# Performance work log

Hardware: AMD Instinct MI355X
Metric: run time of the kernel (lower is better)

The kernel has to match this reference:

```python
import jax, jax.numpy as jnp
import numpy as np

EMBED_DIM = 1024
N_HEADS = 16
HEAD_DIM = EMBED_DIM // N_HEADS
CHUNK = 64  # reward_data_gen_params['chunk_size']
B, T = 8, 1024


def setup_inputs() -> dict:
    key = jax.random.key(0)
    ks = jax.random.split(key, 9)
    s = 0.02
    return {
        "x": jax.random.normal(ks[0], (B, T, EMBED_DIM), dtype=jnp.float32),
        "Wq": jax.random.normal(ks[1], (EMBED_DIM, EMBED_DIM), dtype=jnp.float32) * s,
        "bq": jax.random.normal(ks[2], (EMBED_DIM,), dtype=jnp.float32) * s,
        "Wk": jax.random.normal(ks[3], (EMBED_DIM, EMBED_DIM), dtype=jnp.float32) * s,
        "bk": jax.random.normal(ks[4], (EMBED_DIM,), dtype=jnp.float32) * s,
        "Wv": jax.random.normal(ks[5], (EMBED_DIM, EMBED_DIM), dtype=jnp.float32) * s,
        "bv": jax.random.normal(ks[6], (EMBED_DIM,), dtype=jnp.float32) * s,
        "Wo": jax.random.normal(ks[7], (EMBED_DIM, EMBED_DIM), dtype=jnp.float32) * s,
        "bo": jax.random.normal(ks[8], (EMBED_DIM,), dtype=jnp.float32) * s,
        "attn_scale": jnp.full((1,), 1.0 / np.sqrt(HEAD_DIM), dtype=jnp.float32),
    }


def reference(x, Wq, bq, Wk, bk, Wv, bv, Wo, bo, attn_scale):
    Bsz, Tlen, C = x.shape
    H, D = N_HEADS, HEAD_DIM
    # torch Linear: y = x @ W.T + b
    q = (x @ Wq.T + bq).reshape(Bsz, Tlen, H, D).transpose(0, 2, 1, 3)  # [B,H,T,D]
    k = (x @ Wk.T + bk).reshape(Bsz, Tlen, H, D).transpose(0, 2, 1, 3)
    v = (x @ Wv.T + bv).reshape(Bsz, Tlen, H, D).transpose(0, 2, 1, 3)

    scores = jnp.einsum("bhqd,bhkd->bhqk", q, k) * attn_scale[0]  # [B,H,T,T]

    # Faithful reproduction of the chunked masking: the source only masks when
    # query-chunk >= key-chunk, which (given key>query implies key-chunk>=query-chunk)
    # reduces to masking key>query ONLY inside diagonal CHUNK x CHUNK blocks.
    idx = jnp.arange(Tlen)
    same_block = (idx[:, None] // CHUNK) == (idx[None, :] // CHUNK)
    mask = (idx[None, :] > idx[:, None]) & same_block  # [T,T] True => masked
    scores = jnp.where(mask[None, None], -jnp.inf, scores)

    w = jax.nn.softmax(scores, axis=-1)
    out = jnp.einsum("bhqk,bhkd->bhqd", w, v)  # [B,H,T,D]
    out = out.transpose(0, 2, 1, 3).reshape(Bsz, Tlen, C)
    return out @ Wo.T + bo
```

## Files before the change

### kernel.cpp

```cpp
#include <hip/hip_runtime.h>


typedef __bf16 bf16;
typedef __bf16 bf16x8 __attribute__((ext_vector_type(8)));
typedef float  f32x4  __attribute__((ext_vector_type(4)));

#define LOG2E 1.44269504088896340736f

__device__ __forceinline__ void async16(const bf16* g, bf16* l) {
  __builtin_amdgcn_global_load_lds(
      (const __attribute__((address_space(1))) void*)g,
      (__attribute__((address_space(3))) void*)l, 16, 0, 0);
}

#if __has_builtin(__builtin_amdgcn_exp2f)
#define EXP2F(x) __builtin_amdgcn_exp2f(x)
#else
#define EXP2F(x) exp2f(x)
#endif

__global__ __launch_bounds__(256) void k_convert(
    const float* __restrict__ x, const float* __restrict__ wq,
    const float* __restrict__ wk, const float* __restrict__ wv,
    const float* __restrict__ wo, bf16* __restrict__ xb, bf16* __restrict__ wb) {
  const int XV = (8192 * 1024) / 4;
  const int WV = (1024 * 1024) / 4;
  int i = blockIdx.x * 256 + threadIdx.x;
  const float4* src;
  bf16* dst;
  if (i < XV) {
    src = (const float4*)x + i;
    dst = xb + (size_t)i * 4;
  } else {
    int j = i - XV;
    int w = j >> 18;
    int r = j & (WV - 1);
    const float* s = (w == 0) ? wq : (w == 1) ? wk : (w == 2) ? wv : wo;
    src = (const float4*)s + r;
    dst = wb + (size_t)w * (1024 * 1024) + (size_t)r * 4;
  }
  float4 f = *src;
  bf16 tmp[4] = {(bf16)f.x, (bf16)f.y, (bf16)f.z, (bf16)f.w};
  *(uint2*)dst = *(uint2*)tmp;
}

__global__ __launch_bounds__(256) void k_gemm_qkv(
    const bf16* __restrict__ A, const bf16* __restrict__ W,
    const float* __restrict__ bq, const float* __restrict__ bk,
    const float* __restrict__ bv, const float* __restrict__ scale_p,
    bf16* __restrict__ qb, bf16* __restrict__ kb, bf16* __restrict__ vb) {
  __shared__ __attribute__((aligned(16))) bf16 As[2][4096];
  __shared__ __attribute__((aligned(16))) bf16 Bs[2][4096];
  const int tid = threadIdx.x, lane = tid & 63, wid = tid >> 6;
  const int quad = lane >> 4, l16 = lane & 15;
  const int wm = (wid & 1) * 64, wn = (wid >> 1) * 64;
  const int tileM = blockIdx.x * 128, tileN = blockIdx.y * 128;

  const int rql = lane >> 2;
  const int lc = (lane & 3) ^ ((lane >> 3) & 3);
  const bf16* Ap = A + (size_t)(tileM + wid * 16 + rql) * 1024 + lc * 8;
  const bf16* Bp = W + (size_t)(tileN + wid * 16 + rql) * 1024 + lc * 8;
  const int wofs = wid * 512;

  f32x4 acc[4][4];
#pragma unroll
  for (int i = 0; i < 4; i++)
#pragma unroll
    for (int j = 0; j < 4; j++) acc[i][j] = (f32x4){0.f, 0.f, 0.f, 0.f};

  async16(Ap, &As[0][wofs]);
  async16(Ap + 64 * 1024, &As[0][2048 + wofs]);
  async16(Bp, &Bs[0][wofs]);
  async16(Bp + 64 * 1024, &Bs[0][2048 + wofs]);

  for (int it = 0; it < 32; it++) {
    const int pp = it & 1;
    __syncthreads();
    if (it < 31) {
      int k0 = (it + 1) * 32;
      async16(Ap + k0, &As[pp ^ 1][wofs]);
      async16(Ap + k0 + 64 * 1024, &As[pp ^ 1][2048 + wofs]);
      async16(Bp + k0, &Bs[pp ^ 1][wofs]);
      async16(Bp + k0 + 64 * 1024, &Bs[pp ^ 1][2048 + wofs]);
    }
    bf16x8 af[4], bfr[4];
#pragma unroll
    for (int i = 0; i < 4; i++) {
      int r = wm + i * 16 + l16;
      af[i] = *(const bf16x8*)&As[pp][r * 32 + ((quad ^ ((r >> 1) & 3)) * 8)];
    }
#pragma unroll
    for (int j = 0; j < 4; j++) {
      int r = wn + j * 16 + l16;
      bfr[j] = *(const bf16x8*)&Bs[pp][r * 32 + ((quad ^ ((r >> 1) & 3)) * 8)];
    }
#pragma unroll
    for (int i = 0; i < 4; i++)
#pragma unroll
      for (int j = 0; j < 4; j++)
        acc[i][j] = __builtin_amdgcn_mfma_f32_16x16x32_bf16(af[i], bfr[j], acc[i][j], 0, 0, 0);
  }

  float qscale = scale_p[0] * LOG2E;
#pragma unroll
  for (int i = 0; i < 4; i++) {
    int m0 = tileM + wm + i * 16 + quad * 4;
    int b = m0 >> 10;
    int t0 = m0 & 1023;
#pragma unroll
    for (int j = 0; j < 4; j++) {
      int n = tileN + wn + j * 16 + l16;
      int which = n >> 10;
      int nm = n & 1023;
      int h = nm >> 6, d = nm & 63;
      float bias = ((which == 0) ? bq : (which == 1) ? bk : bv)[nm];
      if (which == 2) {
        bf16 tmp[4];
#pragma unroll
        for (int r = 0; r < 4; r++) tmp[r] = (bf16)(acc[i][j][r] + bias);
        size_t vidx = (((size_t)((b * 16 + h) * 64 + d)) << 10) | (size_t)t0;
        *(uint2*)&vb[vidx] = *(uint2*)tmp;
      } else {
#pragma unroll
        for (int r = 0; r < 4; r++) {
          float v = acc[i][j][r] + bias;
          size_t idx = (((size_t)(b * 16 + h) * 1024 + (t0 + r)) << 6) | (size_t)d;
          if (which == 0) qb[idx] = (bf16)(v * qscale);
          else            kb[idx] = (bf16)v;
        }
      }
    }
  }
}

__global__ __launch_bounds__(256) void k_gemm_out(
    const bf16* __restrict__ A, const bf16* __restrict__ W,
    const float* __restrict__ bo, float* __restrict__ out) {
  __shared__ __attribute__((aligned(16))) bf16 As[2][4096];
  __shared__ __attribute__((aligned(16))) bf16 Bs[2][4096];
  const int tid = threadIdx.x, lane = tid & 63, wid = tid >> 6;
  const int quad = lane >> 4, l16 = lane & 15;
  const int wm = (wid & 1) * 64, wn = (wid >> 1) * 64;
  const int tileM = blockIdx.x * 128, tileN = blockIdx.y * 128;

  const int rql = lane >> 2;
  const int lc = (lane & 3) ^ ((lane >> 3) & 3);
  const bf16* Ap = A + (size_t)(tileM + wid * 16 + rql) * 1024 + lc * 8;
  const bf16* Bp = W + (size_t)(tileN + wid * 16 + rql) * 1024 + lc * 8;
  const int wofs = wid * 512;

  f32x4 acc[4][4];
#pragma unroll
  for (int i = 0; i < 4; i++)
#pragma unroll
    for (int j = 0; j < 4; j++) acc[i][j] = (f32x4){0.f, 0.f, 0.f, 0.f};

  async16(Ap, &As[0][wofs]);
  async16(Ap + 64 * 1024, &As[0][2048 + wofs]);
  async16(Bp, &Bs[0][wofs]);
  async16(Bp + 64 * 1024, &Bs[0][2048 + wofs]);

  for (int it = 0; it < 32; it++) {
    const int pp = it & 1;
    __syncthreads();
    if (it < 31) {
      int k0 = (it + 1) * 32;
      async16(Ap + k0, &As[pp ^ 1][wofs]);
      async16(Ap + k0 + 64 * 1024, &As[pp ^ 1][2048 + wofs]);
      async16(Bp + k0, &Bs[pp ^ 1][wofs]);
      async16(Bp + k0 + 64 * 1024, &Bs[pp ^ 1][2048 + wofs]);
    }
    bf16x8 af[4], bfr[4];
#pragma unroll
    for (int i = 0; i < 4; i++) {
      int r = wm + i * 16 + l16;
      af[i] = *(const bf16x8*)&As[pp][r * 32 + ((quad ^ ((r >> 1) & 3)) * 8)];
    }
#pragma unroll
    for (int j = 0; j < 4; j++) {
      int r = wn + j * 16 + l16;
      bfr[j] = *(const bf16x8*)&Bs[pp][r * 32 + ((quad ^ ((r >> 1) & 3)) * 8)];
    }
#pragma unroll
    for (int i = 0; i < 4; i++)
#pragma unroll
      for (int j = 0; j < 4; j++)
        acc[i][j] = __builtin_amdgcn_mfma_f32_16x16x32_bf16(af[i], bfr[j], acc[i][j], 0, 0, 0);
  }

#pragma unroll
  for (int i = 0; i < 4; i++)
#pragma unroll
    for (int j = 0; j < 4; j++) {
      int n = tileN + wn + j * 16 + l16;
      float bias = bo[n];
#pragma unroll
      for (int r = 0; r < 4; r++) {
        int m = tileM + wm + i * 16 + quad * 4 + r;
        out[(size_t)m * 1024 + n] = acc[i][j][r] + bias;
      }
    }
}

__global__ __launch_bounds__(256, 2) void k_attn(
    const bf16* __restrict__ qb, const bf16* __restrict__ kb,
    const bf16* __restrict__ vb, bf16* __restrict__ attn) {
  __shared__ __attribute__((aligned(16))) bf16 KsF[2][4096];
  __shared__ __attribute__((aligned(16))) bf16 VsF[2][4096];
  __shared__ __attribute__((aligned(16))) bf16 Pl[4][4][16][72];
  const int tid = threadIdx.x, lane = tid & 63, wid = tid >> 6;
  const int quad = lane >> 4, l16 = lane & 15;
  const int bh = blockIdx.x;
  const int qt = blockIdx.y;
  const size_t base = (size_t)bh * (1024 * 64);
  const int qrow0 = qt * 256;

  bf16x8 qf[4][2];
#pragma unroll
  for (int s = 0; s < 4; s++) {
    const bf16* qrow = qb + base + (size_t)(qrow0 + s * 64 + wid * 16 + l16) * 64;
    qf[s][0] = *(const bf16x8*)(qrow + quad * 8);
    qf[s][1] = *(const bf16x8*)(qrow + 32 + quad * 8);
  }

  f32x4 oacc[4][4], lacc[4];
#pragma unroll
  for (int s = 0; s < 4; s++) {
    lacc[s] = (f32x4){0.f, 0.f, 0.f, 0.f};
#pragma unroll
    for (int j = 0; j < 4; j++) oacc[s][j] = (f32x4){0.f, 0.f, 0.f, 0.f};
  }

  bf16x8 ones;
#pragma unroll
  for (int e = 0; e < 8; e++) ones[e] = (bf16)1.0f;

  const int krow = lane >> 3;
  const int klc = (lane & 7) ^ krow;
  const bf16* kp = kb + base + (size_t)(wid * 8 + krow) * 64 + klc * 8;
  const bf16* vp = vb + base + (size_t)(wid * 8 + krow) * 1024 + klc * 8;
  const int wofs = wid * 512;

  async16(kp, &KsF[0][wofs]);
  async16(kp + 32 * 64, &KsF[0][2048 + wofs]);
  async16(vp, &VsF[0][wofs]);
  async16(vp + 32 * 1024, &VsF[0][2048 + wofs]);

  const int sw = l16 & 7;
  for (int kt = 0; kt < 16; kt++) {
    const int pp = kt & 1;
    __syncthreads();

    if (kt < 15) {
      const bf16* kpn = kp + (size_t)(kt + 1) * 4096;
      const bf16* vpn = vp + (size_t)(kt + 1) * 64;
      async16(kpn, &KsF[pp ^ 1][wofs]);
      async16(kpn + 32 * 64, &KsF[pp ^ 1][2048 + wofs]);
      async16(vpn, &VsF[pp ^ 1][wofs]);
      async16(vpn + 32 * 1024, &VsF[pp ^ 1][2048 + wofs]);
    }

    bf16x8 kf[4][2];
#pragma unroll
    for (int j = 0; j < 4; j++) {
      int row = (j * 16 + l16) * 64;
      kf[j][0] = *(const bf16x8*)&KsF[pp][row + ((quad ^ sw) * 8)];
      kf[j][1] = *(const bf16x8*)&KsF[pp][row + (((quad + 4) ^ sw) * 8)];
    }
#pragma unroll
    for (int s = 0; s < 4; s++) {
      f32x4 sv[4];
#pragma unroll
      for (int j = 0; j < 4; j++) {
        f32x4 z = (f32x4){0.f, 0.f, 0.f, 0.f};
        z = __builtin_amdgcn_mfma_f32_16x16x32_bf16(qf[s][0], kf[j][0], z, 0, 0, 0);
        z = __builtin_amdgcn_mfma_f32_16x16x32_bf16(qf[s][1], kf[j][1], z, 0, 0, 0);
        sv[j] = z;
      }
      if (qt * 4 + s == kt) {
#pragma unroll
        for (int j = 0; j < 4; j++) {
          int kpos = j * 16 + l16;
#pragma unroll
          for (int r = 0; r < 4; r++) {
            int qpos = wid * 16 + quad * 4 + r;
            if (kpos > qpos) sv[j][r] = -1e30f;
          }
        }
      }
#pragma unroll
      for (int j = 0; j < 4; j++)
#pragma unroll
        for (int r = 0; r < 4; r++)
          Pl[wid][s][quad * 4 + r][j * 16 + l16] = (bf16)EXP2F(sv[j][r]);
    }

#pragma unroll
    for (int ks = 0; ks < 2; ks++) {
      bf16x8 vf[4];
#pragma unroll
      for (int j = 0; j < 4; j++) {
        int row = (j * 16 + l16) * 64;
        vf[j] = *(const bf16x8*)&VsF[pp][row + (((ks * 4 + quad) ^ sw) * 8)];
      }
#pragma unroll
      for (int s = 0; s < 4; s++) {
        bf16x8 pf = *(const bf16x8*)&Pl[wid][s][l16][ks * 32 + quad * 8];
#pragma unroll
        for (int j = 0; j < 4; j++)
          oacc[s][j] = __builtin_amdgcn_mfma_f32_16x16x32_bf16(pf, vf[j], oacc[s][j], 0, 0, 0);
        lacc[s] = __builtin_amdgcn_mfma_f32_16x16x32_bf16(pf, ones, lacc[s], 0, 0, 0);
      }
    }
  }

  const int b = bh >> 4, h = bh & 15;
#pragma unroll
  for (int s = 0; s < 4; s++) {
    float inv[4];
#pragma unroll
    for (int r = 0; r < 4; r++) inv[r] = 1.0f / lacc[s][r];
#pragma unroll
    for (int j = 0; j < 4; j++)
#pragma unroll
      for (int r = 0; r < 4; r++) {
        int qg = qrow0 + s * 64 + wid * 16 + quad * 4 + r;
        float o = oacc[s][j][r] * inv[r];
        attn[((size_t)(b * 1024 + qg) << 10) + h * 64 + j * 16 + l16] = (bf16)o;
      }
  }
}

extern "C" void kernel_launch(void* const* d_in, const int* in_sizes, int n_in,
                              void* d_out, int out_size, void* d_ws, size_t ws_size,
                              hipStream_t stream) {
  const float* x     = (const float*)d_in[0];
  const float* Wq    = (const float*)d_in[1];
  const float* bq    = (const float*)d_in[2];
  const float* Wk    = (const float*)d_in[3];
  const float* bk    = (const float*)d_in[4];
  const float* Wv    = (const float*)d_in[5];
  const float* bv    = (const float*)d_in[6];
  const float* Wo    = (const float*)d_in[7];
  const float* bo    = (const float*)d_in[8];
  const float* scale = (const float*)d_in[9];

  char* ws = (char*)d_ws;
  bf16* xb   = (bf16*)(ws);
  bf16* wb   = (bf16*)(ws + (size_t)(16 << 20));
  bf16* qb   = (bf16*)(ws + (size_t)(24 << 20));
  bf16* kb   = (bf16*)(ws + (size_t)(40 << 20));
  bf16* vb   = (bf16*)(ws + (size_t)(56 << 20));
  bf16* attn = xb;
  float* out = (float*)d_out;

  hipLaunchKernelGGL(k_convert, dim3(12288), dim3(256), 0, stream,
                     x, Wq, Wk, Wv, Wo, xb, wb);
  hipLaunchKernelGGL(k_gemm_qkv, dim3(64, 24), dim3(256), 0, stream,
                     xb, wb, bq, bk, bv, scale, qb, kb, vb);
  hipLaunchKernelGGL(k_attn, dim3(128, 4), dim3(256), 0, stream,
                     qb, kb, vb, attn);
  hipLaunchKernelGGL(k_gemm_out, dim3(64, 8), dim3(256), 0, stream,
                     attn, wb + (size_t)3072 * 1024, bo, out);
}
```

Baseline: 252.6 us.

## Keep attention P in registers via transposed MFMA and widen GEMM K-tile

The attention kernel now computes S^T by swapping the MFMA operands. The exponentiated probabilities then land directly in the B-operand register layout for the PV product. This removes the shared-memory P round trip and the extra ones-MFMA used for row sums, which are replaced by register sums plus cross-lane shuffles, and the output stores become 4-wide. The two GEMMs switch from a double-buffered 32-wide K tile to a single-buffered 64-wide K tile with two barriers per iteration, which removes prefetch overlap in exchange for fewer iterations and a new swizzle.

```diff
diff --git a/kernel.cpp b/kernel.cpp
--- a/kernel.cpp
+++ b/kernel.cpp
@@ -2,6 +2,7 @@
 
 
 typedef __bf16 bf16;
+typedef __bf16 bf16x4 __attribute__((ext_vector_type(4)));
 typedef __bf16 bf16x8 __attribute__((ext_vector_type(8)));
 typedef float  f32x4  __attribute__((ext_vector_type(4)));
 
@@ -49,18 +50,19 @@
     const float* __restrict__ bq, const float* __restrict__ bk,
     const float* __restrict__ bv, const float* __restrict__ scale_p,
     bf16* __restrict__ qb, bf16* __restrict__ kb, bf16* __restrict__ vb) {
-  __shared__ __attribute__((aligned(16))) bf16 As[2][4096];
-  __shared__ __attribute__((aligned(16))) bf16 Bs[2][4096];
+  __shared__ __attribute__((aligned(16))) bf16 As[8192];
+  __shared__ __attribute__((aligned(16))) bf16 Bs[8192];
   const int tid = threadIdx.x, lane = tid & 63, wid = tid >> 6;
   const int quad = lane >> 4, l16 = lane & 15;
   const int wm = (wid & 1) * 64, wn = (wid >> 1) * 64;
   const int tileM = blockIdx.x * 128, tileN = blockIdx.y * 128;
 
-  const int rql = lane >> 2;
-  const int lc = (lane & 3) ^ ((lane >> 3) & 3);
-  const bf16* Ap = A + (size_t)(tileM + wid * 16 + rql) * 1024 + lc * 8;
-  const bf16* Bp = W + (size_t)(tileN + wid * 16 + rql) * 1024 + lc * 8;
+  const int krow = lane >> 3;
+  const int gc = (lane & 7) ^ krow;
+  const bf16* Ap = A + (size_t)(tileM + wid * 8 + krow) * 1024 + gc * 8;
+  const bf16* Bp = W + (size_t)(tileN + wid * 8 + krow) * 1024 + gc * 8;
   const int wofs = wid * 512;
+  const int s7 = l16 & 7;
 
   f32x4 acc[4][4];
 #pragma unroll
@@ -68,37 +70,31 @@
 #pragma unroll
     for (int j = 0; j < 4; j++) acc[i][j] = (f32x4){0.f, 0.f, 0.f, 0.f};
 
-  async16(Ap, &As[0][wofs]);
-  async16(Ap + 64 * 1024, &As[0][2048 + wofs]);
-  async16(Bp, &Bs[0][wofs]);
-  async16(Bp + 64 * 1024, &Bs[0][2048 + wofs]);
-
-  for (int it = 0; it < 32; it++) {
-    const int pp = it & 1;
-    __syncthreads();
-    if (it < 31) {
-      int k0 = (it + 1) * 32;
-      async16(Ap + k0, &As[pp ^ 1][wofs]);
-      async16(Ap + k0 + 64 * 1024, &As[pp ^ 1][2048 + wofs]);
-      async16(Bp + k0, &Bs[pp ^ 1][wofs]);
-      async16(Bp + k0 + 64 * 1024, &Bs[pp ^ 1][2048 + wofs]);
-    }
-    bf16x8 af[4], bfr[4];
-#pragma unroll
-    for (int i = 0; i < 4; i++) {
-      int r = wm + i * 16 + l16;
-      af[i] = *(const bf16x8*)&As[pp][r * 32 + ((quad ^ ((r >> 1) & 3)) * 8)];
-    }
-#pragma unroll
-    for (int j = 0; j < 4; j++) {
-      int r = wn + j * 16 + l16;
-      bfr[j] = *(const bf16x8*)&Bs[pp][r * 32 + ((quad ^ ((r >> 1) & 3)) * 8)];
-    }
-#pragma unroll
-    for (int i = 0; i < 4; i++)
+  for (int it = 0; it < 16; it++) {
+    const int k0 = it * 64;
+#pragma unroll
+    for (int rd = 0; rd < 4; rd++) {
+      async16(Ap + (size_t)rd * 32768 + k0, &As[rd * 2048 + wofs]);
+      async16(Bp + (size_t)rd * 32768 + k0, &Bs[rd * 2048 + wofs]);
+    }
+    __syncthreads();
+#pragma unroll
+    for (int kh = 0; kh < 2; kh++) {
+      const int pc = ((kh * 4 + quad) ^ s7) * 8;
+      bf16x8 af[4], bfr[4];
+#pragma unroll
+      for (int i = 0; i < 4; i++)
+        af[i] = *(const bf16x8*)&As[(wm + i * 16 + l16) * 64 + pc];
 #pragma unroll
       for (int j = 0; j < 4; j++)
-        acc[i][j] = __builtin_amdgcn_mfma_f32_16x16x32_bf16(af[i], bfr[j], acc[i][j], 0, 0, 0);
+        bfr[j] = *(const bf16x8*)&Bs[(wn + j * 16 + l16) * 64 + pc];
+#pragma unroll
+      for (int i = 0; i < 4; i++)
+#pragma unroll
+        for (int j = 0; j < 4; j++)
+          acc[i][j] = __builtin_amdgcn_mfma_f32_16x16x32_bf16(af[i], bfr[j], acc[i][j], 0, 0, 0);
+    }
+    __syncthreads();
   }
 
   float qscale = scale_p[0] * LOG2E;
@@ -136,18 +132,19 @@
 __global__ __launch_bounds__(256) void k_gemm_out(
     const bf16* __restrict__ A, const bf16* __restrict__ W,
     const float* __restrict__ bo, float* __restrict__ out) {
-  __shared__ __attribute__((aligned(16))) bf16 As[2][4096];
-  __shared__ __attribute__((aligned(16))) bf16 Bs[2][4096];
+  __shared__ __attribute__((aligned(16))) bf16 As[8192];
+  __shared__ __attribute__((aligned(16))) bf16 Bs[8192];
   const int tid = threadIdx.x, lane = tid & 63, wid = tid >> 6;
   const int quad = lane >> 4, l16 = lane & 15;
   const int wm = (wid & 1) * 64, wn = (wid >> 1) * 64;
   const int tileM = blockIdx.x * 128, tileN = blockIdx.y * 128;
 
-  const int rql = lane >> 2;
-  const int lc = (lane & 3) ^ ((lane >> 3) & 3);
-  const bf16* Ap = A + (size_t)(tileM + wid * 16 + rql) * 1024 + lc * 8;
-  const bf16* Bp = W + (size_t)(tileN + wid * 16 + rql) * 1024 + lc * 8;
+  const int krow = lane >> 3;
+  const int gc = (lane & 7) ^ krow;
+  const bf16* Ap = A + (size_t)(tileM + wid * 8 + krow) * 1024 + gc * 8;
+  const bf16* Bp = W + (size_t)(tileN + wid * 8 + krow) * 1024 + gc * 8;
   const int wofs = wid * 512;
+  const int s7 = l16 & 7;
 
   f32x4 acc[4][4];
 #pragma unroll
@@ -155,37 +152,31 @@
 #pragma unroll
     for (int j = 0; j < 4; j++) acc[i][j] = (f32x4){0.f, 0.f, 0.f, 0.f};
 
-  async16(Ap, &As[0][wofs]);
-  async16(Ap + 64 * 1024, &As[0][2048 + wofs]);
-  async16(Bp, &Bs[0][wofs]);
-  async16(Bp + 64 * 1024, &Bs[0][2048 + wofs]);
-
-  for (int it = 0; it < 32; it++) {
-    const int pp = it & 1;
-    __syncthreads();
-    if (it < 31) {
-      int k0 = (it + 1) * 32;
-      async16(Ap + k0, &As[pp ^ 1][wofs]);
-      async16(Ap + k0 + 64 * 1024, &As[pp ^ 1][2048 + wofs]);
-      async16(Bp + k0, &Bs[pp ^ 1][wofs]);
-      async16(Bp + k0 + 64 * 1024, &Bs[pp ^ 1][2048 + wofs]);
-    }
-    bf16x8 af[4], bfr[4];
-#pragma unroll
-    for (int i = 0; i < 4; i++) {
-      int r = wm + i * 16 + l16;
-      af[i] = *(const bf16x8*)&As[pp][r * 32 + ((quad ^ ((r >> 1) & 3)) * 8)];
-    }
-#pragma unroll
-    for (int j = 0; j < 4; j++) {
-      int r = wn + j * 16 + l16;
-      bfr[j] = *(const bf16x8*)&Bs[pp][r * 32 + ((quad ^ ((r >> 1) & 3)) * 8)];
-    }
-#pragma unroll
-    for (int i = 0; i < 4; i++)
+  for (int it = 0; it < 16; it++) {
+    const int k0 = it * 64;
+#pragma unroll
+    for (int rd = 0; rd < 4; rd++) {
+      async16(Ap + (size_t)rd * 32768 + k0, &As[rd * 2048 + wofs]);
+      async16(Bp + (size_t)rd * 32768 + k0, &Bs[rd * 2048 + wofs]);
+    }
+    __syncthreads();
+#pragma unroll
+    for (int kh = 0; kh < 2; kh++) {
+      const int pc = ((kh * 4 + quad) ^ s7) * 8;
+      bf16x8 af[4], bfr[4];
+#pragma unroll
+      for (int i = 0; i < 4; i++)
+        af[i] = *(const bf16x8*)&As[(wm + i * 16 + l16) * 64 + pc];
 #pragma unroll
       for (int j = 0; j < 4; j++)
-        acc[i][j] = __builtin_amdgcn_mfma_f32_16x16x32_bf16(af[i], bfr[j], acc[i][j], 0, 0, 0);
+        bfr[j] = *(const bf16x8*)&Bs[(wn + j * 16 + l16) * 64 + pc];
+#pragma unroll
+      for (int i = 0; i < 4; i++)
+#pragma unroll
+        for (int j = 0; j < 4; j++)
+          acc[i][j] = __builtin_amdgcn_mfma_f32_16x16x32_bf16(af[i], bfr[j], acc[i][j], 0, 0, 0);
+    }
+    __syncthreads();
   }
 
 #pragma unroll
@@ -207,7 +198,6 @@
     const bf16* __restrict__ vb, bf16* __restrict__ attn) {
   __shared__ __attribute__((aligned(16))) bf16 KsF[2][4096];
   __shared__ __attribute__((aligned(16))) bf16 VsF[2][4096];
-  __shared__ __attribute__((aligned(16))) bf16 Pl[4][4][16][72];
   const int tid = threadIdx.x, lane = tid & 63, wid = tid >> 6;
   const int quad = lane >> 4, l16 = lane & 15;
   const int bh = blockIdx.x;
@@ -223,17 +213,14 @@
     qf[s][1] = *(const bf16x8*)(qrow + 32 + quad * 8);
   }
 
-  f32x4 oacc[4][4], lacc[4];
+  f32x4 oacc[4][4];
+  float lpart[4];
 #pragma unroll
   for (int s = 0; s < 4; s++) {
-    lacc[s] = (f32x4){0.f, 0.f, 0.f, 0.f};
-#pragma unroll
-    for (int j = 0; j < 4; j++) oacc[s][j] = (f32x4){0.f, 0.f, 0.f, 0.f};
-  }
-
-  bf16x8 ones;
-#pragma unroll
-  for (int e = 0; e < 8; e++) ones[e] = (bf16)1.0f;
+    lpart[s] = 0.f;
+#pragma unroll
+    for (int n = 0; n < 4; n++) oacc[s][n] = (f32x4){0.f, 0.f, 0.f, 0.f};
+  }
 
   const int krow = lane >> 3;
   const int klc = (lane & 7) ^ krow;
@@ -247,6 +234,7 @@
   async16(vp + 32 * 1024, &VsF[0][2048 + wofs]);
 
   const int sw = l16 & 7;
+  const int qpos16 = wid * 16 + l16;
   for (int kt = 0; kt < 16; kt++) {
     const int pp = kt & 1;
     __syncthreads();
@@ -267,67 +255,78 @@
       kf[j][0] = *(const bf16x8*)&KsF[pp][row + ((quad ^ sw) * 8)];
       kf[j][1] = *(const bf16x8*)&KsF[pp][row + (((quad + 4) ^ sw) * 8)];
     }
+    bf16x8 pfrag[4][2];
 #pragma unroll
     for (int s = 0; s < 4; s++) {
       f32x4 sv[4];
 #pragma unroll
       for (int j = 0; j < 4; j++) {
         f32x4 z = (f32x4){0.f, 0.f, 0.f, 0.f};
-        z = __builtin_amdgcn_mfma_f32_16x16x32_bf16(qf[s][0], kf[j][0], z, 0, 0, 0);
-        z = __builtin_amdgcn_mfma_f32_16x16x32_bf16(qf[s][1], kf[j][1], z, 0, 0, 0);
+        z = __builtin_amdgcn_mfma_f32_16x16x32_bf16(kf[j][0], qf[s][0], z, 0, 0, 0);
+        z = __builtin_amdgcn_mfma_f32_16x16x32_bf16(kf[j][1], qf[s][1], z, 0, 0, 0);
         sv[j] = z;
       }
       if (qt * 4 + s == kt) {
 #pragma unroll
         for (int j = 0; j < 4; j++) {
-          int kpos = j * 16 + l16;
+          int kbase = j * 16 + quad * 4;
+#pragma unroll
+          for (int r = 0; r < 4; r++)
+            if (kbase + r > qpos16) sv[j][r] = -1e30f;
+        }
+      }
+#pragma unroll
+      for (int t = 0; t < 2; t++) {
+        union { bf16x8 v; bf16 e[8]; } pu;
+#pragma unroll
+        for (int j2 = 0; j2 < 2; j2++)
 #pragma unroll
           for (int r = 0; r < 4; r++) {
-            int qpos = wid * 16 + quad * 4 + r;
-            if (kpos > qpos) sv[j][r] = -1e30f;
+            float p = EXP2F(sv[t * 2 + j2][r]);
+            lpart[s] += p;
+            pu.e[j2 * 4 + r] = (bf16)p;
           }
-        }
-      }
-#pragma unroll
-      for (int j = 0; j < 4; j++)
-#pragma unroll
-        for (int r = 0; r < 4; r++)
-          Pl[wid][s][quad * 4 + r][j * 16 + l16] = (bf16)EXP2F(sv[j][r]);
-    }
-
-#pragma unroll
-    for (int ks = 0; ks < 2; ks++) {
+        pfrag[s][t] = pu.v;
+      }
+    }
+
+#pragma unroll
+    for (int t = 0; t < 2; t++) {
       bf16x8 vf[4];
 #pragma unroll
-      for (int j = 0; j < 4; j++) {
-        int row = (j * 16 + l16) * 64;
-        vf[j] = *(const bf16x8*)&VsF[pp][row + (((ks * 4 + quad) ^ sw) * 8)];
-      }
-#pragma unroll
-      for (int s = 0; s < 4; s++) {
-        bf16x8 pf = *(const bf16x8*)&Pl[wid][s][l16][ks * 32 + quad * 8];
-#pragma unroll
-        for (int j = 0; j < 4; j++)
-          oacc[s][j] = __builtin_amdgcn_mfma_f32_16x16x32_bf16(pf, vf[j], oacc[s][j], 0, 0, 0);
-        lacc[s] = __builtin_amdgcn_mfma_f32_16x16x32_bf16(pf, ones, lacc[s], 0, 0, 0);
-      }
+      for (int n = 0; n < 4; n++) {
+        int rb = (n * 16 + l16) * 64;
+        int g1 = 4 * t + (quad >> 1);
+        int off = (quad & 1) * 4;
+        union { bf16x8 v; bf16x4 h[2]; } u;
+        u.h[0] = *(const bf16x4*)&VsF[pp][rb + ((g1 ^ sw) * 8) + off];
+        u.h[1] = *(const bf16x4*)&VsF[pp][rb + (((g1 + 2) ^ sw) * 8) + off];
+        vf[n] = u.v;
+      }
+#pragma unroll
+      for (int s = 0; s < 4; s++)
+#pragma unroll
+        for (int n = 0; n < 4; n++)
+          oacc[s][n] = __builtin_amdgcn_mfma_f32_16x16x32_bf16(vf[n], pfrag[s][t], oacc[s][n], 0, 0, 0);
     }
   }
 
   const int b = bh >> 4, h = bh & 15;
 #pragma unroll
   for (int s = 0; s < 4; s++) {
-    float inv[4];
-#pragma unroll
-    for (int r = 0; r < 4; r++) inv[r] = 1.0f / lacc[s][r];
-#pragma unroll
-    for (int j = 0; j < 4; j++)
-#pragma unroll
-      for (int r = 0; r < 4; r++) {
-        int qg = qrow0 + s * 64 + wid * 16 + quad * 4 + r;
-        float o = oacc[s][j][r] * inv[r];
-        attn[((size_t)(b * 1024 + qg) << 10) + h * 64 + j * 16 + l16] = (bf16)o;
-      }
+    float l = lpart[s];
+    l += __shfl_xor(l, 16, 64);
+    l += __shfl_xor(l, 32, 64);
+    float inv = 1.0f / l;
+    int t = qrow0 + s * 64 + wid * 16 + l16;
+    size_t rowb = ((size_t)(b * 1024 + t) << 10) + h * 64 + quad * 4;
+#pragma unroll
+    for (int n = 0; n < 4; n++) {
+      bf16 tmp[4];
+#pragma unroll
+      for (int r = 0; r < 4; r++) tmp[r] = (bf16)(oacc[s][n][r] * inv);
+      *(uint2*)&attn[rowb + n * 16] = *(uint2*)tmp;
+    }
   }
 }
 
```

New measurement: 231.3 us. -8.5%, faster.
